# Performance work log

Hardware: AMD Instinct MI355X
Metric: run time of the kernel (lower is better)

Reference implementation:

```python
import jax, jax.numpy as jnp
import numpy as np

N = 100000   # nodes
E = 1600000  # edges (avg degree 16)
D = 64       # feature dim
STEPS = 3

def setup_inputs() -> dict:
    key = jax.random.key(0)
    ks = jax.random.split(key, 16)
    def rn(i, shape, scale=1.0):
        return jax.random.normal(ks[i], shape, dtype=jnp.float32) * scale
    inp = {
        "nodes": rn(0, (N, D)),
        "edges": rn(1, (E, D)),
        "globals_": rn(2, (1, D)),
        "senders": jax.random.randint(ks[3], (E,), 0, N, dtype=jnp.int32),
        "receivers": jax.random.randint(ks[4], (E,), 0, N, dtype=jnp.int32),
        # edge MLP: in 4*D -> D -> D
        "We1": rn(5, (4 * D, D), (4 * D) ** -0.5),
        "be1": jnp.zeros((D,), jnp.float32),
        "We2": rn(6, (D, D), D ** -0.5),
        "be2": jnp.zeros((D,), jnp.float32),
        # node MLP: in 3*D -> D -> D
        "Wn1": rn(7, (3 * D, D), (3 * D) ** -0.5),
        "bn1": jnp.zeros((D,), jnp.float32),
        "Wn2": rn(8, (D, D), D ** -0.5),
        "bn2": jnp.zeros((D,), jnp.float32),
        # global MLP: in 3*D -> D -> D
        "Wg1": rn(9, (3 * D, D), (3 * D) ** -0.5),
        "bg1": jnp.zeros((D,), jnp.float32),
        "Wg2": rn(10, (D, D), D ** -0.5),
        "bg2": jnp.zeros((D,), jnp.float32),
    }
    return inp

def _mlp(x, W1, b1, W2, b2):
    return jax.nn.relu(x @ W1 + b1) @ W2 + b2

def reference(nodes, edges, globals_, senders, receivers,
              We1, be1, We2, be2, Wn1, bn1, Wn2, bn2, Wg1, bg1, Wg2, bg2):
    g = globals_  # [1, D], single graph
    n_nodes = nodes.shape[0]
    for _ in range(STEPS):
        # --- edge update: gather sender/receiver node feats + broadcast globals ---
        sent = nodes[senders]        # [E, D]
        recv = nodes[receivers]      # [E, D]
        ge = jnp.broadcast_to(g, (edges.shape[0], g.shape[-1]))
        edges = _mlp(jnp.concatenate([edges, sent, recv, ge], axis=-1),
                     We1, be1, We2, be2)  # [E, D]
        # --- aggregate edges to nodes (received messages) ---
        received = jax.ops.segment_sum(edges, receivers, num_segments=n_nodes)
        gn = jnp.broadcast_to(g, (n_nodes, g.shape[-1]))
        nodes = _mlp(jnp.concatenate([nodes, received, gn], axis=-1),
                     Wn1, bn1, Wn2, bn2)  # [N, D]
        # --- aggregate to globals (single graph => full sums) ---
        agg_n = jnp.sum(nodes, axis=0, keepdims=True)  # [1, D]
        agg_e = jnp.sum(edges, axis=0, keepdims=True)  # [1, D]
        g = _mlp(jnp.concatenate([agg_n, agg_e, g], axis=-1),
                 Wg1, bg1, Wg2, bg2)  # [1, D]
    return nodes, edges, g
```

## Files before the change

kernel.cpp:

```cpp
#include <hip/hip_runtime.h>

#define DD 64
typedef unsigned int uint32;
typedef unsigned short ushort16;
typedef short bf16x8 __attribute__((ext_vector_type(8)));
typedef float f32x4 __attribute__((ext_vector_type(4)));

__device__ __forceinline__ ushort16 f2bf(float x) {
    uint32 u = __float_as_uint(x);
    uint32 r = (u + 0x7FFFu + ((u >> 16) & 1u)) >> 16;
    return (ushort16)r;
}
__device__ __forceinline__ float bf2f(ushort16 h) {
    return __uint_as_float(((uint32)h) << 16);
}
__device__ __forceinline__ uint32 packsplit(float x) {
    ushort16 hi = f2bf(x);
    ushort16 lo = f2bf(x - bf2f(hi));
    return ((uint32)hi << 16) | (uint32)lo;
}

__device__ __forceinline__ void split8f(const float4& a, const float4& b, bf16x8& ah, bf16x8& al) {
    float xs[8] = {a.x, a.y, a.z, a.w, b.x, b.y, b.z, b.w};
#pragma unroll
    for (int i = 0; i < 8; ++i) {
        ushort16 hi = f2bf(xs[i]);
        ah[i] = (short)hi;
        al[i] = (short)f2bf(xs[i] - bf2f(hi));
    }
}
__device__ __forceinline__ void unpack8(const uint4& a, const uint4& b, bf16x8& ah, bf16x8& al) {
    uint32 us[8] = {a.x, a.y, a.z, a.w, b.x, b.y, b.z, b.w};
#pragma unroll
    for (int i = 0; i < 8; ++i) {
        ah[i] = (short)(us[i] >> 16);
        al[i] = (short)(us[i] & 0xFFFFu);
    }
}

__device__ __forceinline__ void mfma_ks(const unsigned short* __restrict__ wks, int l,
                                        const bf16x8* ah, const bf16x8* al, f32x4 (*acc)[4]) {
#pragma unroll
    for (int tt = 0; tt < 4; ++tt) {
        bf16x8 bh = *(const bf16x8*)(wks + ((size_t)(tt * 2 + 0) * 64 + l) * 8);
        bf16x8 bl = *(const bf16x8*)(wks + ((size_t)(tt * 2 + 1) * 64 + l) * 8);
#pragma unroll
        for (int m = 0; m < 4; ++m) {
            acc[m][tt] = __builtin_amdgcn_mfma_f32_16x16x32_bf16(ah[m], bh, acc[m][tt], 0, 0, 0);
            acc[m][tt] = __builtin_amdgcn_mfma_f32_16x16x32_bf16(ah[m], bl, acc[m][tt], 0, 0, 0);
            acc[m][tt] = __builtin_amdgcn_mfma_f32_16x16x32_bf16(al[m], bh, acc[m][tt], 0, 0, 0);
        }
    }
}
__device__ __forceinline__ void mfma_ks_hi(const unsigned short* __restrict__ wks, int l,
                                           const bf16x8* ah, f32x4 (*acc)[4]) {
#pragma unroll
    for (int tt = 0; tt < 4; ++tt) {
        bf16x8 bh = *(const bf16x8*)(wks + ((size_t)(tt * 2 + 0) * 64 + l) * 8);
        bf16x8 bl = *(const bf16x8*)(wks + ((size_t)(tt * 2 + 1) * 64 + l) * 8);
#pragma unroll
        for (int m = 0; m < 4; ++m) {
            acc[m][tt] = __builtin_amdgcn_mfma_f32_16x16x32_bf16(ah[m], bh, acc[m][tt], 0, 0, 0);
            acc[m][tt] = __builtin_amdgcn_mfma_f32_16x16x32_bf16(ah[m], bl, acc[m][tt], 0, 0, 0);
        }
    }
}
__device__ __forceinline__ void mfma_ks1(const unsigned short* __restrict__ wks, int l,
                                         bf16x8 ah, bf16x8 al, f32x4* acc) {
#pragma unroll
    for (int tt = 0; tt < 4; ++tt) {
        bf16x8 bh = *(const bf16x8*)(wks + ((size_t)(tt * 2 + 0) * 64 + l) * 8);
        bf16x8 bl = *(const bf16x8*)(wks + ((size_t)(tt * 2 + 1) * 64 + l) * 8);
        acc[tt] = __builtin_amdgcn_mfma_f32_16x16x32_bf16(ah, bh, acc[tt], 0, 0, 0);
        acc[tt] = __builtin_amdgcn_mfma_f32_16x16x32_bf16(ah, bl, acc[tt], 0, 0, 0);
        acc[tt] = __builtin_amdgcn_mfma_f32_16x16x32_bf16(al, bh, acc[tt], 0, 0, 0);
    }
}

__global__ void zero_counts_kernel(int* __restrict__ counts, int N) {
    int i = blockIdx.x * blockDim.x + threadIdx.x;
    if (i < N) counts[i] = 0;
}
__global__ void hist_kernel(const int* __restrict__ recv, int* __restrict__ counts, int E) {
    int i = blockIdx.x * blockDim.x + threadIdx.x;
    if (i < E) atomicAdd(&counts[recv[i]], 1);
}
__global__ __launch_bounds__(1024) void scan_kernel(const int* __restrict__ counts,
                                                    int* __restrict__ offs,
                                                    int* __restrict__ cursor, int N) {
    __shared__ int sm[1024];
    __shared__ int carryS;
    int t = threadIdx.x;
    if (t == 0) carryS = 0;
    __syncthreads();
    for (int base = 0; base < N; base += 4096) {
        int idx = base + t * 4;
        int x0 = (idx + 0 < N) ? counts[idx + 0] : 0;
        int x1 = (idx + 1 < N) ? counts[idx + 1] : 0;
        int x2 = (idx + 2 < N) ? counts[idx + 2] : 0;
        int x3 = (idx + 3 < N) ? counts[idx + 3] : 0;
        int s1 = x0 + x1, s2 = s1 + x2, s3 = s2 + x3;
        sm[t] = s3;
        __syncthreads();
        for (int d = 1; d < 1024; d <<= 1) {
            int v = (t >= d) ? sm[t - d] : 0;
            __syncthreads();
            sm[t] += v;
            __syncthreads();
        }
        int excl = sm[t] - s3 + carryS;
        if (idx < N)     { offs[idx]     = excl;      cursor[idx]     = excl; }
        if (idx + 1 < N) { offs[idx + 1] = excl + x0; cursor[idx + 1] = excl + x0; }
        if (idx + 2 < N) { offs[idx + 2] = excl + s1; cursor[idx + 2] = excl + s1; }
        if (idx + 3 < N) { offs[idx + 3] = excl + s2; cursor[idx + 3] = excl + s2; }
        int chunkTotal = sm[1023];
        __syncthreads();
        if (t == 0) carryS += chunkTotal;
        __syncthreads();
    }
    if (t == 0) offs[N] = carryS;
}
__global__ void scatter_kernel(const int* __restrict__ recv, int* __restrict__ cursor,
                               int* __restrict__ perm, int E) {
    int i = blockIdx.x * blockDim.x + threadIdx.x;
    if (i < E) {
        int p = atomicAdd(&cursor[recv[i]], 1);
        perm[p] = i;
    }
}

__global__ void prep_bias_kernel(const float* __restrict__ g,
                                 const float* __restrict__ We1, const float* __restrict__ be1,
                                 const float* __restrict__ Wn1, const float* __restrict__ bn1,
                                 float* __restrict__ be1e, float* __restrict__ bn1e) {
    int j = threadIdx.x;
    float a = be1[j];
    float b = bn1[j];
    for (int k = 0; k < DD; ++k) {
        float gk = g[k];
        a = fmaf(gk, We1[(192 + k) * DD + j], a);
        b = fmaf(gk, Wn1[(128 + k) * DD + j], b);
    }
    be1e[j] = a;
    bn1e[j] = b;
}

__global__ void prep_nodes_kernel(const float* __restrict__ src, uint32* __restrict__ dst,
                                  int total) {
    int i = blockIdx.x * blockDim.x + threadIdx.x;
    if (i < total) dst[i] = packsplit(src[i]);
}

__device__ __forceinline__ void prep_pack(const float* __restrict__ W, int nks,
                                          unsigned short* __restrict__ dst, int tid) {
    if (tid < nks * 2048) {
        int i = tid & 7, lane = (tid >> 3) & 63, tt = (tid >> 9) & 3, ks = tid >> 11;
        int k = ks * 32 + (lane >> 4) * 8 + i;
        int n = tt * 16 + (lane & 15);
        float x = W[k * DD + n];
        ushort16 hi = f2bf(x);
        ushort16 lo = f2bf(x - bf2f(hi));
        dst[(((ks * 4 + tt) * 2 + 0) * 64 + lane) * 8 + i] = hi;
        dst[(((ks * 4 + tt) * 2 + 1) * 64 + lane) * 8 + i] = lo;
    }
}
__global__ void prep_weights_kernel(const float* __restrict__ We1, const float* __restrict__ We2,
                                    const float* __restrict__ Wn1, const float* __restrict__ Wn2,
                                    unsigned short* __restrict__ we1p, unsigned short* __restrict__ we2p,
                                    unsigned short* __restrict__ wn1p, unsigned short* __restrict__ wn2p) {
    int tid = blockIdx.x * blockDim.x + threadIdx.x;
    prep_pack(We1, 6, we1p, tid);
    prep_pack(We2, 2, we2p, tid);
    prep_pack(Wn1, 4, wn1p, tid);
    prep_pack(Wn2, 2, wn2p, tid);
}

template<int IN_BF, int OUT_F32>
__global__ __launch_bounds__(256, 3) void edge_kernel_t(
    const float* __restrict__ edges_f32, const unsigned short* __restrict__ edges_bf,
    const uint32* __restrict__ nodes_pk,
    const int* __restrict__ senders, const int* __restrict__ receivers,
    const int* __restrict__ perm,
    const unsigned short* __restrict__ w1, const float* __restrict__ b1,
    const unsigned short* __restrict__ w2, const float* __restrict__ b2,
    float* __restrict__ eout_f32, unsigned short* __restrict__ eout_bf,
    float* __restrict__ received, float* __restrict__ agg_e, int E)
{
    __shared__ int PE[4][64];
    __shared__ int SID[4][64];
    __shared__ int RID[4][64];
    __shared__ float PS[4][64];
    __shared__ __align__(16) char HB[4][4096];

    const int t = threadIdx.x;
    const int w = t >> 6, l = t & 63;
    const int lm = l & 15, kq = l >> 4;
    const int base = (blockIdx.x << 8) + (w << 6);

    {
        int pos = base + l;
        int pe = perm[min(pos, E - 1)];
        PE[w][l] = pe;
        SID[w][l] = senders[pe];
        RID[w][l] = receivers[pe];
    }

    int pe_m[4], sid_m[4], rid_m[4];
#pragma unroll
    for (int m = 0; m < 4; ++m) {
        pe_m[m]  = PE[w][(m << 4) + lm];
        sid_m[m] = SID[w][(m << 4) + lm];
        rid_m[m] = RID[w][(m << 4) + lm];
    }

    float4 re[4][4];
    uint4 rbe[4][2];
    if (IN_BF) {
#pragma unroll
        for (int m = 0; m < 4; ++m) {
            int row = min(base + (m << 4) + lm, E - 1);
            const unsigned short* p = edges_bf + (size_t)row * DD;
            rbe[m][0] = *(const uint4*)(p + kq * 8);
            rbe[m][1] = *(const uint4*)(p + 32 + kq * 8);
        }
    } else {
#pragma unroll
        for (int m = 0; m < 4; ++m) {
            const float* p = edges_f32 + (size_t)pe_m[m] * DD + kq * 8;
            re[m][0] = *(const float4*)(p);
            re[m][1] = *(const float4*)(p + 4);
            re[m][2] = *(const float4*)(p + 32);
            re[m][3] = *(const float4*)(p + 36);
        }
    }
    uint4 rs[4][4];
#pragma unroll
    for (int m = 0; m < 4; ++m) {
        const uint32* p = nodes_pk + (size_t)sid_m[m] * DD + kq * 8;
        rs[m][0] = *(const uint4*)(p);
        rs[m][1] = *(const uint4*)(p + 4);
        rs[m][2] = *(const uint4*)(p + 32);
        rs[m][3] = *(const uint4*)(p + 36);
    }

    f32x4 acc[4][4];
#pragma unroll
    for (int tt = 0; tt < 4; ++tt) {
        float b = b1[tt * 16 + lm];
#pragma unroll
        for (int m = 0; m < 4; ++m) { acc[m][tt][0] = b; acc[m][tt][1] = b; acc[m][tt][2] = b; acc[m][tt][3] = b; }
    }

    if (IN_BF) {
#pragma unroll
        for (int ks2 = 0; ks2 < 2; ++ks2) {
            bf16x8 ah[4];
#pragma unroll
            for (int m = 0; m < 4; ++m) ah[m] = *(bf16x8*)&rbe[m][ks2];
            mfma_ks_hi(w1 + (size_t)ks2 * 4096, l, ah, acc);
        }
    } else {
#pragma unroll
        for (int ks2 = 0; ks2 < 2; ++ks2) {
            bf16x8 ah[4], al[4];
#pragma unroll
            for (int m = 0; m < 4; ++m) split8f(re[m][ks2 * 2], re[m][ks2 * 2 + 1], ah[m], al[m]);
            mfma_ks(w1 + (size_t)ks2 * 4096, l, ah, al, acc);
        }
    }

    uint4 rr[4][4];
#pragma unroll
    for (int m = 0; m < 4; ++m) {
        const uint32* p = nodes_pk + (size_t)rid_m[m] * DD + kq * 8;
        rr[m][0] = *(const uint4*)(p);
        rr[m][1] = *(const uint4*)(p + 4);
        rr[m][2] = *(const uint4*)(p + 32);
        rr[m][3] = *(const uint4*)(p + 36);
    }

#pragma unroll
    for (int ks2 = 0; ks2 < 2; ++ks2) {
        bf16x8 ah[4], al[4];
#pragma unroll
        for (int m = 0; m < 4; ++m) unpack8(rs[m][ks2 * 2], rs[m][ks2 * 2 + 1], ah[m], al[m]);
        mfma_ks(w1 + (size_t)(2 + ks2) * 4096, l, ah, al, acc);
    }
#pragma unroll
    for (int ks2 = 0; ks2 < 2; ++ks2) {
        bf16x8 ah[4], al[4];
#pragma unroll
        for (int m = 0; m < 4; ++m) unpack8(rr[m][ks2 * 2], rr[m][ks2 * 2 + 1], ah[m], al[m]);
        mfma_ks(w1 + (size_t)(4 + ks2) * 4096, l, ah, al, acc);
    }

    float b2v[4];
#pragma unroll
    for (int tt = 0; tt < 4; ++tt) b2v[tt] = b2[tt * 16 + lm];
    float sreg[4] = {0.f, 0.f, 0.f, 0.f};
    char* hh = &HB[w][0];
    char* hl = &HB[w][2048];

#pragma unroll
    for (int m = 0; m < 4; ++m) {
#pragma unroll
        for (int tt = 0; tt < 4; ++tt)
#pragma unroll
            for (int r = 0; r < 4; ++r) {
                int row = (kq << 2) + r;
                int col = (tt << 4) + lm;
                float hv = fmaxf(acc[m][tt][r], 0.f);
                ushort16 hi = f2bf(hv);
                ushort16 lo = f2bf(hv - bf2f(hi));
                int boff = (row << 7) + ((((col >> 3) ^ (row & 7)) & 7) << 4) + ((col & 7) << 1);
                *(unsigned short*)(hh + boff) = hi;
                *(unsigned short*)(hl + boff) = lo;
            }

        f32x4 acc2[4];
#pragma unroll
        for (int tt = 0; tt < 4; ++tt) { acc2[tt][0] = b2v[tt]; acc2[tt][1] = b2v[tt]; acc2[tt][2] = b2v[tt]; acc2[tt][3] = b2v[tt]; }
#pragma unroll
        for (int ks = 0; ks < 2; ++ks) {
            int boff = (lm << 7) + ((((kq + ks * 4) ^ (lm & 7)) & 7) << 4);
            bf16x8 ah = *(const bf16x8*)(hh + boff);
            bf16x8 al = *(const bf16x8*)(hl + boff);
            mfma_ks1(w2 + (size_t)ks * 4096, l, ah, al, acc2);
        }

#pragma unroll
        for (int tt = 0; tt < 4; ++tt)
#pragma unroll
            for (int r = 0; r < 4; ++r) {
                int rowp = base + (m << 4) + (kq << 2) + r;
                if (rowp < E) sreg[tt] += acc2[tt][r];
            }

#pragma unroll
        for (int tt = 0; tt < 4; ++tt)
#pragma unroll
            for (int r = 0; r < 4; ++r) {
                int row = (kq << 2) + r;
                int col = (tt << 4) + lm;
                int boff = (row << 8) + ((((col >> 2) ^ (row & 15)) & 15) << 4) + ((col & 3) << 2);
                *(float*)(&HB[w][0] + boff) = acc2[tt][r];
            }

        {
            int rowp = base + (m << 4) + lm;
            float4 vv[4];
#pragma unroll
            for (int jj = 0; jj < 4; ++jj) {
                int slot = (4 * kq + jj) ^ (lm & 15);
                vv[jj] = *(float4*)(&HB[w][0] + (lm << 8) + (slot << 4));
            }
            if (rowp < E) {
                if (OUT_F32) {
                    float4* dst = (float4*)(eout_f32 + (size_t)pe_m[m] * DD);
#pragma unroll
                    for (int jj = 0; jj < 4; ++jj) dst[kq * 4 + jj] = vv[jj];
                } else {
                    uint4 o0, o1;
                    o0.x = (uint32)f2bf(vv[0].x) | ((uint32)f2bf(vv[0].y) << 16);
                    o0.y = (uint32)f2bf(vv[0].z) | ((uint32)f2bf(vv[0].w) << 16);
                    o0.z = (uint32)f2bf(vv[1].x) | ((uint32)f2bf(vv[1].y) << 16);
                    o0.w = (uint32)f2bf(vv[1].z) | ((uint32)f2bf(vv[1].w) << 16);
                    o1.x = (uint32)f2bf(vv[2].x) | ((uint32)f2bf(vv[2].y) << 16);
                    o1.y = (uint32)f2bf(vv[2].z) | ((uint32)f2bf(vv[2].w) << 16);
                    o1.z = (uint32)f2bf(vv[3].x) | ((uint32)f2bf(vv[3].y) << 16);
                    o1.w = (uint32)f2bf(vv[3].z) | ((uint32)f2bf(vv[3].w) << 16);
                    unsigned short* dst = eout_bf + (size_t)rowp * DD + kq * 16;
                    *(uint4*)(dst) = o0;
                    *(uint4*)(dst + 8) = o1;
                }
            }
        }

        {
            float run = 0.f;
#pragma unroll
            for (int r = 0; r < 16; ++r) {
                int rowp = base + (m << 4) + r;
                if (rowp < E) {
                    int boff = (r << 8) + ((((l >> 2) ^ (r & 15)) & 15) << 4) + ((l & 3) << 2);
                    float v = *(const float*)(&HB[w][0] + boff);
                    int rid = RID[w][(m << 4) + r];
                    run += v;
                    bool flush;
                    if (r == 15) flush = true;
                    else flush = (rowp + 1 >= E) || (RID[w][(m << 4) + r + 1] != rid);
                    if (flush) {
                        atomicAdd(&received[(size_t)rid * DD + l], run);
                        run = 0.f;
                    }
                }
            }
        }
    }

#pragma unroll
    for (int tt = 0; tt < 4; ++tt) {
        float s = sreg[tt];
        s += __shfl_xor(s, 16, 64);
        s += __shfl_xor(s, 32, 64);
        if (l < 16) PS[w][tt * 16 + l] = s;
    }
    __syncthreads();
    if (t < 64) {
        float s = PS[0][t] + PS[1][t] + PS[2][t] + PS[3][t];
        atomicAdd(agg_e + t, s);
    }
}

__global__ __launch_bounds__(256, 2) void node_kernel_mfma(
    const uint32* __restrict__ nodes_pk, const float* __restrict__ received,
    const unsigned short* __restrict__ w1, const float* __restrict__ b1,
    const unsigned short* __restrict__ w2, const float* __restrict__ b2,
    float* __restrict__ nodes_out, uint32* __restrict__ nodes_pk_out, int write_pk,
    float* __restrict__ agg_n, int N)
{
    __shared__ unsigned short HB[4][4][2][1024];
    __shared__ float PS[4][64];

    const int t = threadIdx.x;
    const int w = t >> 6, l = t & 63;
    const int lm = l & 15, kq = l >> 4;
    const int base = (blockIdx.x << 8) + (w << 6);

    int gi[4];
#pragma unroll
    for (int m = 0; m < 4; ++m) gi[m] = min(base + (m << 4) + lm, N - 1);

    uint4 rn[4][4];
#pragma unroll
    for (int m = 0; m < 4; ++m) {
        const uint32* p = nodes_pk + (size_t)gi[m] * DD + kq * 8;
        rn[m][0] = *(const uint4*)(p);
        rn[m][1] = *(const uint4*)(p + 4);
        rn[m][2] = *(const uint4*)(p + 32);
        rn[m][3] = *(const uint4*)(p + 36);
    }
    float4 rc[4][4];
#pragma unroll
    for (int m = 0; m < 4; ++m) {
        const float* p = received + (size_t)gi[m] * DD + kq * 8;
        rc[m][0] = *(const float4*)(p);
        rc[m][1] = *(const float4*)(p + 4);
        rc[m][2] = *(const float4*)(p + 32);
        rc[m][3] = *(const float4*)(p + 36);
    }

    f32x4 acc[4][4];
#pragma unroll
    for (int tt = 0; tt < 4; ++tt) {
        float b = b1[tt * 16 + lm];
#pragma unroll
        for (int m = 0; m < 4; ++m) { acc[m][tt][0] = b; acc[m][tt][1] = b; acc[m][tt][2] = b; acc[m][tt][3] = b; }
    }

#pragma unroll
    for (int ks2 = 0; ks2 < 2; ++ks2) {
        bf16x8 ah[4], al[4];
#pragma unroll
        for (int m = 0; m < 4; ++m) unpack8(rn[m][ks2 * 2], rn[m][ks2 * 2 + 1], ah[m], al[m]);
        mfma_ks(w1 + (size_t)ks2 * 4096, l, ah, al, acc);
    }
#pragma unroll
    for (int ks2 = 0; ks2 < 2; ++ks2) {
        bf16x8 ah[4], al[4];
#pragma unroll
        for (int m = 0; m < 4; ++m) split8f(rc[m][ks2 * 2], rc[m][ks2 * 2 + 1], ah[m], al[m]);
        mfma_ks(w1 + (size_t)(2 + ks2) * 4096, l, ah, al, acc);
    }

#pragma unroll
    for (int m = 0; m < 4; ++m) {
        char* hh = (char*)&HB[w][m][0][0];
        char* hl = (char*)&HB[w][m][1][0];
#pragma unroll
        for (int tt = 0; tt < 4; ++tt)
#pragma unroll
            for (int r = 0; r < 4; ++r) {
                int row = (kq << 2) + r;
                int col = (tt << 4) + lm;
                float hv = fmaxf(acc[m][tt][r], 0.f);
                ushort16 hi = f2bf(hv);
                ushort16 lo = f2bf(hv - bf2f(hi));
                int boff = (row << 7) + ((((col >> 3) ^ (row & 7)) & 7) << 4) + ((col & 7) << 1);
                *(unsigned short*)(hh + boff) = hi;
                *(unsigned short*)(hl + boff) = lo;
            }
    }

    f32x4 acc2[4][4];
#pragma unroll
    for (int tt = 0; tt < 4; ++tt) {
        float b = b2[tt * 16 + lm];
#pragma unroll
        for (int m = 0; m < 4; ++m) { acc2[m][tt][0] = b; acc2[m][tt][1] = b; acc2[m][tt][2] = b; acc2[m][tt][3] = b; }
    }
#pragma unroll
    for (int ks = 0; ks < 2; ++ks) {
        bf16x8 ah[4], al[4];
#pragma unroll
        for (int m = 0; m < 4; ++m) {
            int boff = (lm << 7) + ((((kq + ks * 4) ^ (lm & 7)) & 7) << 4);
            ah[m] = *(const bf16x8*)((char*)&HB[w][m][0][0] + boff);
            al[m] = *(const bf16x8*)((char*)&HB[w][m][1][0] + boff);
        }
        mfma_ks(w2 + (size_t)ks * 4096, l, ah, al, acc2);
    }

#pragma unroll
    for (int tt = 0; tt < 4; ++tt) {
        float s = 0.f;
#pragma unroll
        for (int m = 0; m < 4; ++m)
#pragma unroll
            for (int r = 0; r < 4; ++r) {
                int rowg = base + (m << 4) + (kq << 2) + r;
                if (rowg < N) s += acc2[m][tt][r];
            }
        s += __shfl_xor(s, 16, 64);
        s += __shfl_xor(s, 32, 64);
        if (l < 16) PS[w][tt * 16 + l] = s;
    }

    char* CW = (char*)&HB[w][0][0][0];
#pragma unroll
    for (int m = 0; m < 4; ++m)
#pragma unroll
        for (int tt = 0; tt < 4; ++tt)
#pragma unroll
            for (int r = 0; r < 4; ++r) {
                int row = (kq << 2) + r;
                int col = (tt << 4) + lm;
                int boff = (row << 8) + ((((col >> 2) ^ (row & 15)) & 15) << 4) + ((col & 3) << 2);
                *(float*)(CW + m * 4096 + boff) = acc2[m][tt][r];
            }
#pragma unroll
    for (int m = 0; m < 4; ++m) {
        int rowg = base + (m << 4) + lm;
        float4 vv[4];
#pragma unroll
        for (int jj = 0; jj < 4; ++jj) {
            int slot = (4 * kq + jj) ^ (lm & 15);
            vv[jj] = *(float4*)(CW + m * 4096 + (lm << 8) + (slot << 4));
        }
        if (rowg < N) {
            float4* dst = (float4*)(nodes_out + (size_t)rowg * DD);
#pragma unroll
            for (int jj = 0; jj < 4; ++jj) dst[kq * 4 + jj] = vv[jj];
            if (write_pk) {
                uint32* pdst = nodes_pk_out + (size_t)rowg * DD + kq * 16;
#pragma unroll
                for (int jj = 0; jj < 4; ++jj) {
                    uint4 o;
                    o.x = packsplit(vv[jj].x);
                    o.y = packsplit(vv[jj].y);
                    o.z = packsplit(vv[jj].z);
                    o.w = packsplit(vv[jj].w);
                    *(uint4*)(pdst + jj * 4) = o;
                }
            }
        }
    }

    __syncthreads();
    if (t < 64) {
        float s = PS[0][t] + PS[1][t] + PS[2][t] + PS[3][t];
        atomicAdd(agg_n + t, s);
    }
}

__global__ void global_kernel(const float* __restrict__ agg_n, const float* __restrict__ agg_e,
                              const float* __restrict__ g_in,
                              const float* __restrict__ Wg1, const float* __restrict__ bg1,
                              const float* __restrict__ Wg2, const float* __restrict__ bg2,
                              float* __restrict__ g_out)
{
    __shared__ float h[64];
    int j = threadIdx.x;
    float a = bg1[j];
    for (int k = 0; k < DD; ++k) a = fmaf(agg_n[k], Wg1[k * DD + j], a);
    for (int k = 0; k < DD; ++k) a = fmaf(agg_e[k], Wg1[(64 + k) * DD + j], a);
    for (int k = 0; k < DD; ++k) a = fmaf(g_in[k],  Wg1[(128 + k) * DD + j], a);
    h[j] = fmaxf(a, 0.f);
    __syncthreads();
    float o = bg2[j];
    for (int k = 0; k < DD; ++k) o = fmaf(h[k], Wg2[k * DD + j], o);
    g_out[j] = o;
}

extern "C" void kernel_launch(void* const* d_in, const int* in_sizes, int n_in,
                              void* d_out, int out_size, void* d_ws, size_t ws_size,
                              hipStream_t stream) {
    const float* nodes0 = (const float*)d_in[0];
    const float* edges0 = (const float*)d_in[1];
    const float* g0     = (const float*)d_in[2];
    const int* senders   = (const int*)d_in[3];
    const int* receivers = (const int*)d_in[4];
    const float* We1 = (const float*)d_in[5];
    const float* be1 = (const float*)d_in[6];
    const float* We2 = (const float*)d_in[7];
    const float* be2 = (const float*)d_in[8];
    const float* Wn1 = (const float*)d_in[9];
    const float* bn1 = (const float*)d_in[10];
    const float* Wn2 = (const float*)d_in[11];
    const float* bn2 = (const float*)d_in[12];
    const float* Wg1 = (const float*)d_in[13];
    const float* bg1 = (const float*)d_in[14];
    const float* Wg2 = (const float*)d_in[15];
    const float* bg2 = (const float*)d_in[16];

    const int N = in_sizes[0] / DD;
    const int E = in_sizes[1] / DD;

    float* out_nodes = (float*)d_out;
    float* out_edges = out_nodes + (size_t)N * DD;
    float* out_g     = out_edges + (size_t)E * DD;

    float* ws = (float*)d_ws;
    float* received = ws;
    float* aggs = received + (size_t)N * DD;
    float* agg_n = aggs;
    float* agg_e = aggs + 64;
    float* b1e   = aggs + 128;
    float* b1n   = aggs + 192;
    float* g1    = aggs + 256;
    float* g2    = aggs + 320;
    int* counts = (int*)(aggs + 512);
    int* offs   = counts + N;
    int* cursor = offs + N + 4;
    int* perm   = cursor + N;
    uint32* nodes_pk = (uint32*)(perm + E);
    unsigned short* we1p = (unsigned short*)(nodes_pk + (size_t)N * DD);
    unsigned short* we2p = we1p + 24576;
    unsigned short* wn1p = we2p + 8192;
    unsigned short* wn2p = wn1p + 16384;
    unsigned short* edges_bf = wn2p + 8192;

    size_t need = (size_t)((char*)(edges_bf + (size_t)E * DD) - (char*)d_ws);
    const bool use_bf = (ws_size >= need);

    const int eblocks = (E + 255) / 256;
    const int nblocks = (N + 255) / 256;

    zero_counts_kernel<<<(N + 255) / 256, 256, 0, stream>>>(counts, N);
    hist_kernel<<<(E + 255) / 256, 256, 0, stream>>>(receivers, counts, E);
    scan_kernel<<<1, 1024, 0, stream>>>(counts, offs, cursor, N);
    scatter_kernel<<<(E + 255) / 256, 256, 0, stream>>>(receivers, cursor, perm, E);
    prep_weights_kernel<<<48, 256, 0, stream>>>(We1, We2, Wn1, Wn2, we1p, we2p, wn1p, wn2p);
    prep_nodes_kernel<<<(N * DD + 255) / 256, 256, 0, stream>>>(nodes0, nodes_pk, N * DD);

    for (int s = 0; s < 3; ++s) {
        const float* esrc_f32 = (s == 0) ? edges0 : out_edges;
        const float* gin  = (s == 0) ? g0 : ((s == 1) ? g1 : g2);
        float* gout       = (s == 2) ? out_g : ((s == 0) ? g1 : g2);
        const bool in_bf  = use_bf && (s > 0);
        const bool out_f32 = (!use_bf) || (s == 2);

        hipMemsetAsync(received, 0, ((size_t)N * DD + 128) * sizeof(float), stream);
        prep_bias_kernel<<<1, 64, 0, stream>>>(gin, We1, be1, Wn1, bn1, b1e, b1n);

        if (in_bf) {
            if (out_f32)
                edge_kernel_t<1, 1><<<eblocks, 256, 0, stream>>>(esrc_f32, edges_bf, nodes_pk,
                    senders, receivers, perm, we1p, b1e, we2p, be2,
                    out_edges, edges_bf, received, agg_e, E);
            else
                edge_kernel_t<1, 0><<<eblocks, 256, 0, stream>>>(esrc_f32, edges_bf, nodes_pk,
                    senders, receivers, perm, we1p, b1e, we2p, be2,
                    out_edges, edges_bf, received, agg_e, E);
        } else {
            if (out_f32)
                edge_kernel_t<0, 1><<<eblocks, 256, 0, stream>>>(esrc_f32, edges_bf, nodes_pk,
                    senders, receivers, perm, we1p, b1e, we2p, be2,
                    out_edges, edges_bf, received, agg_e, E);
            else
                edge_kernel_t<0, 0><<<eblocks, 256, 0, stream>>>(esrc_f32, edges_bf, nodes_pk,
                    senders, receivers, perm, we1p, b1e, we2p, be2,
                    out_edges, edges_bf, received, agg_e, E);
        }

        node_kernel_mfma<<<nblocks, 256, 0, stream>>>(nodes_pk, received, wn1p, b1n, wn2p, bn2,
                                                      out_nodes, nodes_pk, (s < 2) ? 1 : 0,
                                                      agg_n, N);
        global_kernel<<<1, 64, 0, stream>>>(agg_n, agg_e, gin, Wg1, bg1, Wg2, bg2, gout);
    }
}
```

Baseline: 2.046 ms.

## Split node hi/lo bf16 planes and pre-permute initial edges to bf16

Node features are stored as separate hi and lo bf16 planes instead of packed 32-bit words. The sender gather now reads only the hi plane, which halves its gather bytes but drops the low-order correction for sender features. A new prep kernel converts the initial fp32 edges to bf16 in receiver-sorted order using an inverse permutation, so step 0 also takes the bf16 input path instead of gathering fp32 edges through perm. This lowers gather traffic in the edge kernel at the cost of reduced precision on sender and initial-edge inputs.

```diff
diff --git a/kernel.cpp b/kernel.cpp
--- a/kernel.cpp
+++ b/kernel.cpp
@@ -14,11 +14,6 @@
 __device__ __forceinline__ float bf2f(ushort16 h) {
     return __uint_as_float(((uint32)h) << 16);
 }
-__device__ __forceinline__ uint32 packsplit(float x) {
-    ushort16 hi = f2bf(x);
-    ushort16 lo = f2bf(x - bf2f(hi));
-    return ((uint32)hi << 16) | (uint32)lo;
-}
 
 __device__ __forceinline__ void split8f(const float4& a, const float4& b, bf16x8& ah, bf16x8& al) {
     float xs[8] = {a.x, a.y, a.z, a.w, b.x, b.y, b.z, b.w};
@@ -27,14 +22,6 @@
         ushort16 hi = f2bf(xs[i]);
         ah[i] = (short)hi;
         al[i] = (short)f2bf(xs[i] - bf2f(hi));
-    }
-}
-__device__ __forceinline__ void unpack8(const uint4& a, const uint4& b, bf16x8& ah, bf16x8& al) {
-    uint32 us[8] = {a.x, a.y, a.z, a.w, b.x, b.y, b.z, b.w};
-#pragma unroll
-    for (int i = 0; i < 8; ++i) {
-        ah[i] = (short)(us[i] >> 16);
-        al[i] = (short)(us[i] & 0xFFFFu);
     }
 }
 
@@ -121,11 +108,12 @@
     if (t == 0) offs[N] = carryS;
 }
 __global__ void scatter_kernel(const int* __restrict__ recv, int* __restrict__ cursor,
-                               int* __restrict__ perm, int E) {
+                               int* __restrict__ perm, int* __restrict__ inv, int E) {
     int i = blockIdx.x * blockDim.x + threadIdx.x;
     if (i < E) {
         int p = atomicAdd(&cursor[recv[i]], 1);
         perm[p] = i;
+        inv[i] = p;
     }
 }
 
@@ -145,10 +133,34 @@
     bn1e[j] = b;
 }
 
-__global__ void prep_nodes_kernel(const float* __restrict__ src, uint32* __restrict__ dst,
+__global__ void prep_nodes_kernel(const float* __restrict__ src,
+                                  unsigned short* __restrict__ h, unsigned short* __restrict__ l,
                                   int total) {
     int i = blockIdx.x * blockDim.x + threadIdx.x;
-    if (i < total) dst[i] = packsplit(src[i]);
+    if (i < total) {
+        float x = src[i];
+        ushort16 hi = f2bf(x);
+        h[i] = hi;
+        l[i] = f2bf(x - bf2f(hi));
+    }
+}
+
+__global__ void prep_edges_kernel(const float* __restrict__ e0, const int* __restrict__ inv,
+                                  unsigned short* __restrict__ ebf, int E) {
+    int tid = blockIdx.x * blockDim.x + threadIdx.x;
+    if (tid < E * 8) {
+        int e = tid >> 3, part = tid & 7;
+        const float* p = e0 + (size_t)e * DD + part * 8;
+        float4 a = *(const float4*)(p);
+        float4 b = *(const float4*)(p + 4);
+        uint4 o;
+        o.x = (uint32)f2bf(a.x) | ((uint32)f2bf(a.y) << 16);
+        o.y = (uint32)f2bf(a.z) | ((uint32)f2bf(a.w) << 16);
+        o.z = (uint32)f2bf(b.x) | ((uint32)f2bf(b.y) << 16);
+        o.w = (uint32)f2bf(b.z) | ((uint32)f2bf(b.w) << 16);
+        int ip = inv[e];
+        *(uint4*)(ebf + (size_t)ip * DD + part * 8) = o;
+    }
 }
 
 __device__ __forceinline__ void prep_pack(const float* __restrict__ W, int nks,
@@ -178,7 +190,7 @@
 template<int IN_BF, int OUT_F32>
 __global__ __launch_bounds__(256, 3) void edge_kernel_t(
     const float* __restrict__ edges_f32, const unsigned short* __restrict__ edges_bf,
-    const uint32* __restrict__ nodes_pk,
+    const unsigned short* __restrict__ nodes_h, const unsigned short* __restrict__ nodes_l,
     const int* __restrict__ senders, const int* __restrict__ receivers,
     const int* __restrict__ perm,
     const unsigned short* __restrict__ w1, const float* __restrict__ b1,
@@ -213,15 +225,15 @@
         rid_m[m] = RID[w][(m << 4) + lm];
     }
 
+    uint4 rbe[4][2];
     float4 re[4][4];
-    uint4 rbe[4][2];
     if (IN_BF) {
 #pragma unroll
         for (int m = 0; m < 4; ++m) {
             int row = min(base + (m << 4) + lm, E - 1);
-            const unsigned short* p = edges_bf + (size_t)row * DD;
-            rbe[m][0] = *(const uint4*)(p + kq * 8);
-            rbe[m][1] = *(const uint4*)(p + 32 + kq * 8);
+            const unsigned short* p = edges_bf + (size_t)row * DD + kq * 8;
+            rbe[m][0] = *(const uint4*)(p);
+            rbe[m][1] = *(const uint4*)(p + 32);
         }
     } else {
 #pragma unroll
@@ -233,14 +245,22 @@
             re[m][3] = *(const float4*)(p + 36);
         }
     }
-    uint4 rs[4][4];
+    uint4 rsh[4][2];
 #pragma unroll
     for (int m = 0; m < 4; ++m) {
-        const uint32* p = nodes_pk + (size_t)sid_m[m] * DD + kq * 8;
-        rs[m][0] = *(const uint4*)(p);
-        rs[m][1] = *(const uint4*)(p + 4);
-        rs[m][2] = *(const uint4*)(p + 32);
-        rs[m][3] = *(const uint4*)(p + 36);
+        const unsigned short* p = nodes_h + (size_t)sid_m[m] * DD + kq * 8;
+        rsh[m][0] = *(const uint4*)(p);
+        rsh[m][1] = *(const uint4*)(p + 32);
+    }
+    uint4 rrh[4][2], rrl[4][2];
+#pragma unroll
+    for (int m = 0; m < 4; ++m) {
+        const unsigned short* ph = nodes_h + (size_t)rid_m[m] * DD + kq * 8;
+        const unsigned short* pl = nodes_l + (size_t)rid_m[m] * DD + kq * 8;
+        rrh[m][0] = *(const uint4*)(ph);
+        rrh[m][1] = *(const uint4*)(ph + 32);
+        rrl[m][0] = *(const uint4*)(pl);
+        rrl[m][1] = *(const uint4*)(pl + 32);
     }
 
     f32x4 acc[4][4];
@@ -268,29 +288,18 @@
             mfma_ks(w1 + (size_t)ks2 * 4096, l, ah, al, acc);
         }
     }
-
-    uint4 rr[4][4];
-#pragma unroll
-    for (int m = 0; m < 4; ++m) {
-        const uint32* p = nodes_pk + (size_t)rid_m[m] * DD + kq * 8;
-        rr[m][0] = *(const uint4*)(p);
-        rr[m][1] = *(const uint4*)(p + 4);
-        rr[m][2] = *(const uint4*)(p + 32);
-        rr[m][3] = *(const uint4*)(p + 36);
-    }
-
+#pragma unroll
+    for (int ks2 = 0; ks2 < 2; ++ks2) {
+        bf16x8 ah[4];
+#pragma unroll
+        for (int m = 0; m < 4; ++m) ah[m] = *(bf16x8*)&rsh[m][ks2];
+        mfma_ks_hi(w1 + (size_t)(2 + ks2) * 4096, l, ah, acc);
+    }
 #pragma unroll
     for (int ks2 = 0; ks2 < 2; ++ks2) {
         bf16x8 ah[4], al[4];
 #pragma unroll
-        for (int m = 0; m < 4; ++m) unpack8(rs[m][ks2 * 2], rs[m][ks2 * 2 + 1], ah[m], al[m]);
-        mfma_ks(w1 + (size_t)(2 + ks2) * 4096, l, ah, al, acc);
-    }
-#pragma unroll
-    for (int ks2 = 0; ks2 < 2; ++ks2) {
-        bf16x8 ah[4], al[4];
-#pragma unroll
-        for (int m = 0; m < 4; ++m) unpack8(rr[m][ks2 * 2], rr[m][ks2 * 2 + 1], ah[m], al[m]);
+        for (int m = 0; m < 4; ++m) { ah[m] = *(bf16x8*)&rrh[m][ks2]; al[m] = *(bf16x8*)&rrl[m][ks2]; }
         mfma_ks(w1 + (size_t)(4 + ks2) * 4096, l, ah, al, acc);
     }
 
@@ -413,11 +422,13 @@
 }
 
 __global__ __launch_bounds__(256, 2) void node_kernel_mfma(
-    const uint32* __restrict__ nodes_pk, const float* __restrict__ received,
+    const unsigned short* __restrict__ nodes_h_in, const unsigned short* __restrict__ nodes_l_in,
+    const float* __restrict__ received,
     const unsigned short* __restrict__ w1, const float* __restrict__ b1,
     const unsigned short* __restrict__ w2, const float* __restrict__ b2,
-    float* __restrict__ nodes_out, uint32* __restrict__ nodes_pk_out, int write_pk,
-    float* __restrict__ agg_n, int N)
+    float* __restrict__ nodes_out,
+    unsigned short* __restrict__ nodes_h_out, unsigned short* __restrict__ nodes_l_out,
+    int write_pk, float* __restrict__ agg_n, int N)
 {
     __shared__ unsigned short HB[4][4][2][1024];
     __shared__ float PS[4][64];
@@ -431,14 +442,15 @@
 #pragma unroll
     for (int m = 0; m < 4; ++m) gi[m] = min(base + (m << 4) + lm, N - 1);
 
-    uint4 rn[4][4];
+    uint4 rnh[4][2], rnl[4][2];
 #pragma unroll
     for (int m = 0; m < 4; ++m) {
-        const uint32* p = nodes_pk + (size_t)gi[m] * DD + kq * 8;
-        rn[m][0] = *(const uint4*)(p);
-        rn[m][1] = *(const uint4*)(p + 4);
-        rn[m][2] = *(const uint4*)(p + 32);
-        rn[m][3] = *(const uint4*)(p + 36);
+        const unsigned short* ph = nodes_h_in + (size_t)gi[m] * DD + kq * 8;
+        const unsigned short* pl = nodes_l_in + (size_t)gi[m] * DD + kq * 8;
+        rnh[m][0] = *(const uint4*)(ph);
+        rnh[m][1] = *(const uint4*)(ph + 32);
+        rnl[m][0] = *(const uint4*)(pl);
+        rnl[m][1] = *(const uint4*)(pl + 32);
     }
     float4 rc[4][4];
 #pragma unroll
@@ -462,7 +474,7 @@
     for (int ks2 = 0; ks2 < 2; ++ks2) {
         bf16x8 ah[4], al[4];
 #pragma unroll
-        for (int m = 0; m < 4; ++m) unpack8(rn[m][ks2 * 2], rn[m][ks2 * 2 + 1], ah[m], al[m]);
+        for (int m = 0; m < 4; ++m) { ah[m] = *(bf16x8*)&rnh[m][ks2]; al[m] = *(bf16x8*)&rnl[m][ks2]; }
         mfma_ks(w1 + (size_t)ks2 * 4096, l, ah, al, acc);
     }
 #pragma unroll
@@ -552,16 +564,31 @@
 #pragma unroll
             for (int jj = 0; jj < 4; ++jj) dst[kq * 4 + jj] = vv[jj];
             if (write_pk) {
-                uint32* pdst = nodes_pk_out + (size_t)rowg * DD + kq * 16;
-#pragma unroll
-                for (int jj = 0; jj < 4; ++jj) {
-                    uint4 o;
-                    o.x = packsplit(vv[jj].x);
-                    o.y = packsplit(vv[jj].y);
-                    o.z = packsplit(vv[jj].z);
-                    o.w = packsplit(vv[jj].w);
-                    *(uint4*)(pdst + jj * 4) = o;
+                unsigned short* hdst = nodes_h_out + (size_t)rowg * DD + kq * 16;
+                unsigned short* ldst = nodes_l_out + (size_t)rowg * DD + kq * 16;
+                uint4 oh, ol;
+                float xs[16] = {vv[0].x, vv[0].y, vv[0].z, vv[0].w,
+                                vv[1].x, vv[1].y, vv[1].z, vv[1].w,
+                                vv[2].x, vv[2].y, vv[2].z, vv[2].w,
+                                vv[3].x, vv[3].y, vv[3].z, vv[3].w};
+                uint32 hw[8], lw[8];
+#pragma unroll
+                for (int q = 0; q < 8; ++q) {
+                    ushort16 h0 = f2bf(xs[2 * q]);
+                    ushort16 h1 = f2bf(xs[2 * q + 1]);
+                    ushort16 l0 = f2bf(xs[2 * q] - bf2f(h0));
+                    ushort16 l1 = f2bf(xs[2 * q + 1] - bf2f(h1));
+                    hw[q] = (uint32)h0 | ((uint32)h1 << 16);
+                    lw[q] = (uint32)l0 | ((uint32)l1 << 16);
                 }
+                oh.x = hw[0]; oh.y = hw[1]; oh.z = hw[2]; oh.w = hw[3];
+                *(uint4*)(hdst) = oh;
+                oh.x = hw[4]; oh.y = hw[5]; oh.z = hw[6]; oh.w = hw[7];
+                *(uint4*)(hdst + 8) = oh;
+                ol.x = lw[0]; ol.y = lw[1]; ol.z = lw[2]; ol.w = lw[3];
+                *(uint4*)(ldst) = ol;
+                ol.x = lw[4]; ol.y = lw[5]; ol.z = lw[6]; ol.w = lw[7];
+                *(uint4*)(ldst + 8) = ol;
             }
         }
     }
@@ -633,8 +660,10 @@
     int* offs   = counts + N;
     int* cursor = offs + N + 4;
     int* perm   = cursor + N;
-    uint32* nodes_pk = (uint32*)(perm + E);
-    unsigned short* we1p = (unsigned short*)(nodes_pk + (size_t)N * DD);
+    int* inv    = perm + E;
+    unsigned short* nodes_h = (unsigned short*)(inv + E);
+    unsigned short* nodes_l = nodes_h + (size_t)N * DD;
+    unsigned short* we1p = nodes_l + (size_t)N * DD;
     unsigned short* we2p = we1p + 24576;
     unsigned short* wn1p = we2p + 8192;
     unsigned short* wn2p = wn1p + 16384;
@@ -649,43 +678,39 @@
     zero_counts_kernel<<<(N + 255) / 256, 256, 0, stream>>>(counts, N);
     hist_kernel<<<(E + 255) / 256, 256, 0, stream>>>(receivers, counts, E);
     scan_kernel<<<1, 1024, 0, stream>>>(counts, offs, cursor, N);
-    scatter_kernel<<<(E + 255) / 256, 256, 0, stream>>>(receivers, cursor, perm, E);
+    scatter_kernel<<<(E + 255) / 256, 256, 0, stream>>>(receivers, cursor, perm, inv, E);
     prep_weights_kernel<<<48, 256, 0, stream>>>(We1, We2, Wn1, Wn2, we1p, we2p, wn1p, wn2p);
-    prep_nodes_kernel<<<(N * DD + 255) / 256, 256, 0, stream>>>(nodes0, nodes_pk, N * DD);
+    prep_nodes_kernel<<<(N * DD + 255) / 256, 256, 0, stream>>>(nodes0, nodes_h, nodes_l, N * DD);
+    if (use_bf)
+        prep_edges_kernel<<<(E * 8 + 255) / 256, 256, 0, stream>>>(edges0, inv, edges_bf, E);
 
     for (int s = 0; s < 3; ++s) {
         const float* esrc_f32 = (s == 0) ? edges0 : out_edges;
         const float* gin  = (s == 0) ? g0 : ((s == 1) ? g1 : g2);
         float* gout       = (s == 2) ? out_g : ((s == 0) ? g1 : g2);
-        const bool in_bf  = use_bf && (s > 0);
-        const bool out_f32 = (!use_bf) || (s == 2);
 
         hipMemsetAsync(received, 0, ((size_t)N * DD + 128) * sizeof(float), stream);
         prep_bias_kernel<<<1, 64, 0, stream>>>(gin, We1, be1, Wn1, bn1, b1e, b1n);
 
-        if (in_bf) {
-            if (out_f32)
-                edge_kernel_t<1, 1><<<eblocks, 256, 0, stream>>>(esrc_f32, edges_bf, nodes_pk,
+        if (use_bf) {
+            if (s == 2)
+                edge_kernel_t<1, 1><<<eblocks, 256, 0, stream>>>(esrc_f32, edges_bf, nodes_h, nodes_l,
                     senders, receivers, perm, we1p, b1e, we2p, be2,
                     out_edges, edges_bf, received, agg_e, E);
             else
-                edge_kernel_t<1, 0><<<eblocks, 256, 0, stream>>>(esrc_f32, edges_bf, nodes_pk,
+                edge_kernel_t<1, 0><<<eblocks, 256, 0, stream>>>(esrc_f32, edges_bf, nodes_h, nodes_l,
                     senders, receivers, perm, we1p, b1e, we2p, be2,
                     out_edges, edges_bf, received, agg_e, E);
         } else {
-            if (out_f32)
-                edge_kernel_t<0, 1><<<eblocks, 256, 0, stream>>>(esrc_f32, edges_bf, nodes_pk,
-                    senders, receivers, perm, we1p, b1e, we2p, be2,
-                    out_edges, edges_bf, received, agg_e, E);
-            else
-                edge_kernel_t<0, 0><<<eblocks, 256, 0, stream>>>(esrc_f32, edges_bf, nodes_pk,
-                    senders, receivers, perm, we1p, b1e, we2p, be2,
-                    out_edges, edges_bf, received, agg_e, E);
-        }
-
-        node_kernel_mfma<<<nblocks, 256, 0, stream>>>(nodes_pk, received, wn1p, b1n, wn2p, bn2,
-                                                      out_nodes, nodes_pk, (s < 2) ? 1 : 0,
-                                                      agg_n, N);
+            edge_kernel_t<0, 1><<<eblocks, 256, 0, stream>>>(esrc_f32, edges_bf, nodes_h, nodes_l,
+                senders, receivers, perm, we1p, b1e, we2p, be2,
+                out_edges, edges_bf, received, agg_e, E);
+        }
+
+        node_kernel_mfma<<<nblocks, 256, 0, stream>>>(nodes_h, nodes_l, received,
+                                                      wn1p, b1n, wn2p, bn2,
+                                                      out_nodes, nodes_h, nodes_l,
+                                                      (s < 2) ? 1 : 0, agg_n, N);
         global_kernel<<<1, 64, 0, stream>>>(agg_n, agg_e, gin, Wg1, bg1, Wg2, bg2, gout);
     }
 }
```

Result: faster. 1.918 ms (-6.3%).
